# Kernel tuning notes

Measured on AMD Instinct MI355X. Metric: run time of the kernel, lower is better.

The kernel has to match this reference:

```python
import jax, jax.numpy as jnp
import numpy as np

UNITS = 50

def setup_inputs() -> dict:
    key = jax.random.key(0)
    ks = jax.random.split(key, 6)
    B, T, F = 4096, 128, 64
    scale = 0.1
    return {
        "x": jax.random.normal(ks[0], (B, T, F), dtype=jnp.float32),
        "W": jax.random.normal(ks[1], (F, 3 * UNITS), dtype=jnp.float32) * scale,
        "U": jax.random.normal(ks[2], (UNITS, 3 * UNITS), dtype=jnp.float32) * scale,
        "b": jax.random.normal(ks[3], (2, 3 * UNITS), dtype=jnp.float32) * scale,
        "Wd": jax.random.normal(ks[4], (UNITS, 1), dtype=jnp.float32) * scale,
        "bd": jnp.zeros((1,), dtype=jnp.float32),
    }

def reference(x, W, U, b, Wd, bd):
    # Keras GRU, reset_after=True, activation=relu, recurrent_activation=sigmoid.
    B, T, F = x.shape
    u = UNITS
    # Precompute input projections for all timesteps: [B,T,3u]
    xp = jnp.einsum('btf,fk->btk', x, W) + b[0]
    xp = jnp.moveaxis(xp, 1, 0)  # [T,B,3u]
    bi = b[1]

    def step(h, xt):
        hp = h @ U + bi                     # [B,3u]
        xz, xr, xh = xt[:, :u], xt[:, u:2*u], xt[:, 2*u:]
        hz, hr, hh = hp[:, :u], hp[:, u:2*u], hp[:, 2*u:]
        z = jax.nn.sigmoid(xz + hz)
        r = jax.nn.sigmoid(xr + hr)
        hcand = jax.nn.relu(xh + r * hh)
        h_new = z * h + (1.0 - z) * hcand
        return h_new, None

    h0 = jnp.zeros((B, u), dtype=x.dtype)
    hT, _ = jax.lax.scan(step, h0, xp)
    # Dropout is identity at inference; Dense head:
    return hT @ Wd + bd
```

## Files before the change

### kernel.cpp

```cpp
#include <hip/hip_runtime.h>
#include <math.h>

typedef _Float16 v8h __attribute__((ext_vector_type(8)));
typedef float v4f __attribute__((ext_vector_type(4)));

#define UNITS    50
#define K3       150
#define FDIM     64
#define TSTEPS   128
#define BATCH    4096
#define NBATCH   16
#define NTHREADS 192
#define HS16_STRIDE 72
#define HS32_STRIDE 52
#define SP_STRIDE   20


__global__ __launch_bounds__(NTHREADS, 1)
void gru_mfma(const float* __restrict__ x, const float* __restrict__ W,
              const float* __restrict__ U, const float* __restrict__ bias,
              const float* __restrict__ Wd, const float* __restrict__ bd,
              float* __restrict__ out) {
    __shared__ float    sPre[4 * 64 * SP_STRIDE];
    __shared__ _Float16 hs16[NBATCH * HS16_STRIDE];
    __shared__ float    hs32[NBATCH * HS32_STRIDE];

    const int tid  = threadIdx.x;
    const int g    = tid >> 6;
    const int lane = tid & 63;
    const int n    = lane & 15;
    const int quad = lane >> 4;
    const int b0   = blockIdx.x * NBATCH;

    for (int i = tid; i < NBATCH * HS16_STRIDE; i += NTHREADS) hs16[i] = (_Float16)0.f;
    for (int i = tid; i < NBATCH * HS32_STRIDE; i += NTHREADS) hs32[i] = 0.f;

    v8h B[4][4];
    #pragma unroll
    for (int kt = 0; kt < 4; ++kt) {
        #pragma unroll
        for (int nt = 0; nt < 4; ++nt) {
            const int c = nt * 16 + n;
            v8h f;
            #pragma unroll
            for (int j = 0; j < 8; ++j) {
                const int k = kt * 32 + quad * 8 + j;
                float v = 0.f;
                if (c < UNITS) {
                    const int gcol = g * UNITS + c;
                    if (k < FDIM)              v = W[k * K3 + gcol];
                    else if (k < FDIM + UNITS) v = U[(k - FDIM) * K3 + gcol];
                }
                f[j] = (_Float16)v;
            }
            B[kt][nt] = f;
        }
    }

    float bZR[4], bX[4], bH[4];
    #pragma unroll
    for (int nt = 0; nt < 4; ++nt) {
        const int c = nt * 16 + n;
        float vzr = 0.f, vx = 0.f, vh = 0.f;
        if (c < UNITS) {
            if (g < 2) vzr = bias[g * UNITS + c] + bias[K3 + g * UNITS + c];
            vx = bias[2 * UNITS + c];
            vh = bias[K3 + 2 * UNITS + c];
        }
        bZR[nt] = vzr; bX[nt] = vx; bH[nt] = vh;
    }

    const float* xbase = x + ((size_t)(b0 + n) * TSTEPS) * FDIM + quad * 8;
    v4f px0 = *(const v4f*)(xbase + 0);
    v4f px1 = *(const v4f*)(xbase + 4);
    v4f px2 = *(const v4f*)(xbase + 32);
    v4f px3 = *(const v4f*)(xbase + 36);

    __syncthreads();

    for (int t = 0; t < TSTEPS; ++t) {
        v8h A0, A1, A2, A3;
        #pragma unroll
        for (int j = 0; j < 4; ++j) {
            A0[j]     = (_Float16)px0[j];
            A0[j + 4] = (_Float16)px1[j];
            A1[j]     = (_Float16)px2[j];
            A1[j + 4] = (_Float16)px3[j];
        }
        A2 = *(const v8h*)(&hs16[n * HS16_STRIDE + quad * 8]);
        A3 = *(const v8h*)(&hs16[n * HS16_STRIDE + 32 + quad * 8]);

        if (t + 1 < TSTEPS) {
            const float* xp = xbase + (size_t)(t + 1) * FDIM;
            px0 = *(const v4f*)(xp + 0);
            px1 = *(const v4f*)(xp + 4);
            px2 = *(const v4f*)(xp + 32);
            px3 = *(const v4f*)(xp + 36);
        }

        if (g < 2) {
            #pragma unroll
            for (int nt = 0; nt < 4; ++nt) {
                v4f acc = {bZR[nt], bZR[nt], bZR[nt], bZR[nt]};
                acc = __builtin_amdgcn_mfma_f32_16x16x32_f16(A0, B[0][nt], acc, 0, 0, 0);
                acc = __builtin_amdgcn_mfma_f32_16x16x32_f16(A1, B[1][nt], acc, 0, 0, 0);
                acc = __builtin_amdgcn_mfma_f32_16x16x32_f16(A2, B[2][nt], acc, 0, 0, 0);
                acc = __builtin_amdgcn_mfma_f32_16x16x32_f16(A3, B[3][nt], acc, 0, 0, 0);
                const int c = nt * 16 + n;
                *(v4f*)(&sPre[(g * 64 + c) * SP_STRIDE + quad * 4]) = acc;
            }
        } else {
            #pragma unroll
            for (int nt = 0; nt < 4; ++nt) {
                v4f ax = {bX[nt], bX[nt], bX[nt], bX[nt]};
                ax = __builtin_amdgcn_mfma_f32_16x16x32_f16(A0, B[0][nt], ax, 0, 0, 0);
                ax = __builtin_amdgcn_mfma_f32_16x16x32_f16(A1, B[1][nt], ax, 0, 0, 0);
                v4f ah = {bH[nt], bH[nt], bH[nt], bH[nt]};
                ah = __builtin_amdgcn_mfma_f32_16x16x32_f16(A2, B[2][nt], ah, 0, 0, 0);
                ah = __builtin_amdgcn_mfma_f32_16x16x32_f16(A3, B[3][nt], ah, 0, 0, 0);
                const int c = nt * 16 + n;
                *(v4f*)(&sPre[(2 * 64 + c) * SP_STRIDE + quad * 4]) = ax;
                *(v4f*)(&sPre[(3 * 64 + c) * SP_STRIDE + quad * 4]) = ah;
            }
        }
        __syncthreads();

        for (int idx = tid; idx < NBATCH * UNITS; idx += NTHREADS) {
            const int u = idx >> 4;
            const int m = idx & 15;
            const float zp = sPre[(0 * 64 + u) * SP_STRIDE + m];
            const float rp = sPre[(1 * 64 + u) * SP_STRIDE + m];
            const float hx = sPre[(2 * 64 + u) * SP_STRIDE + m];
            const float hh = sPre[(3 * 64 + u) * SP_STRIDE + m];
            const float z  = 1.f / (1.f + __expf(-zp));
            const float r  = 1.f / (1.f + __expf(-rp));
            const float hc = fmaxf(fmaf(r, hh, hx), 0.f);
            const float ho = hs32[m * HS32_STRIDE + u];
            const float hn = fmaf(z, ho - hc, hc);
            hs32[m * HS32_STRIDE + u] = hn;
            hs16[m * HS16_STRIDE + u] = (_Float16)hn;
        }
        __syncthreads();
    }

    if (tid < NBATCH) {
        float acc = bd[0];
        #pragma unroll
        for (int u = 0; u < UNITS; ++u)
            acc = fmaf(hs32[tid * HS32_STRIDE + u], Wd[u], acc);
        out[b0 + tid] = acc;
    }
}

extern "C" void kernel_launch(void* const* d_in, const int* in_sizes, int n_in,
                              void* d_out, int out_size, void* d_ws, size_t ws_size,
                              hipStream_t stream) {
    const float* x    = (const float*)d_in[0];
    const float* W    = (const float*)d_in[1];
    const float* U    = (const float*)d_in[2];
    const float* bias = (const float*)d_in[3];
    const float* Wd   = (const float*)d_in[4];
    const float* bd   = (const float*)d_in[5];
    float* out = (float*)d_out;

    dim3 grid(BATCH / NBATCH);
    dim3 block(NTHREADS);
    gru_mfma<<<grid, block, 0, stream>>>(x, W, U, bias, Wd, bd, out);
}
```

Baseline: 308.3 us.

## Run each GRU batch tile in a single wave with register-resident gates

Collapses the three-wave block into one 64-lane wave that computes all z, r and h gate MFMAs and applies the GRU update directly on the accumulator registers. This removes the shared-memory pre-activation staging and one barrier per timestep. The hidden state now stays in fp32 registers, and the recurrent h-bias is folded into the weight matrix through a constant-one column in the fp16 state. The sigmoids use exp2 and a single shared reciprocal. The trade-off is roughly three times more MFMA work per wave and many more weight registers (48 v8h), which risks register pressure and longer serial MFMA chains per block.

```diff
diff --git a/kernel.cpp b/kernel.cpp
--- a/kernel.cpp
+++ b/kernel.cpp
@@ -9,77 +9,97 @@
 #define FDIM     64
 #define TSTEPS   128
 #define BATCH    4096
-#define NBATCH   16
-#define NTHREADS 192
-#define HS16_STRIDE 72
-#define HS32_STRIDE 52
-#define SP_STRIDE   20
+#define NB       16
+#define H16S     72
+#define H32S     52
 
+#if __has_builtin(__builtin_amdgcn_exp2f)
+__device__ __forceinline__ float fast_exp2(float x) { return __builtin_amdgcn_exp2f(x); }
+#else
+__device__ __forceinline__ float fast_exp2(float x) { return exp2f(x); }
+#endif
+#if __has_builtin(__builtin_amdgcn_rcpf)
+__device__ __forceinline__ float fast_rcp(float x) { return __builtin_amdgcn_rcpf(x); }
+#else
+__device__ __forceinline__ float fast_rcp(float x) { return 1.0f / x; }
+#endif
 
-__global__ __launch_bounds__(NTHREADS, 1)
-void gru_mfma(const float* __restrict__ x, const float* __restrict__ W,
-              const float* __restrict__ U, const float* __restrict__ bias,
+__global__ __launch_bounds__(64, 1)
+void gru_wave(const float* __restrict__ x, const float* __restrict__ W,
+              const float* __restrict__ U, const float* __restrict__ bv,
               const float* __restrict__ Wd, const float* __restrict__ bd,
               float* __restrict__ out) {
-    __shared__ float    sPre[4 * 64 * SP_STRIDE];
-    __shared__ _Float16 hs16[NBATCH * HS16_STRIDE];
-    __shared__ float    hs32[NBATCH * HS32_STRIDE];
+    __shared__ _Float16 hs16[NB * H16S];
+    __shared__ float    hs32[NB * H32S];
 
-    const int tid  = threadIdx.x;
-    const int g    = tid >> 6;
-    const int lane = tid & 63;
+    const int lane = threadIdx.x;
     const int n    = lane & 15;
     const int quad = lane >> 4;
-    const int b0   = blockIdx.x * NBATCH;
+    const int b0   = blockIdx.x * NB;
 
-    for (int i = tid; i < NBATCH * HS16_STRIDE; i += NTHREADS) hs16[i] = (_Float16)0.f;
-    for (int i = tid; i < NBATCH * HS32_STRIDE; i += NTHREADS) hs32[i] = 0.f;
+    for (int i = lane; i < NB * H16S; i += 64) hs16[i] = (_Float16)0.f;
+    __syncthreads();
+    if (lane < NB) hs16[lane * H16S + 50] = (_Float16)1.f;
 
-    v8h B[4][4];
+    v8h Bz[4][4], Br[4][4], Bh[4][4];
     #pragma unroll
     for (int kt = 0; kt < 4; ++kt) {
         #pragma unroll
         for (int nt = 0; nt < 4; ++nt) {
             const int c = nt * 16 + n;
-            v8h f;
+            v8h fz, fr, fh;
             #pragma unroll
             for (int j = 0; j < 8; ++j) {
                 const int k = kt * 32 + quad * 8 + j;
-                float v = 0.f;
+                float vz = 0.f, vr = 0.f, vh = 0.f;
                 if (c < UNITS) {
-                    const int gcol = g * UNITS + c;
-                    if (k < FDIM)              v = W[k * K3 + gcol];
-                    else if (k < FDIM + UNITS) v = U[(k - FDIM) * K3 + gcol];
+                    if (k < FDIM) {
+                        vz = W[k * K3 + c];
+                        vr = W[k * K3 + 50 + c];
+                        vh = W[k * K3 + 100 + c];
+                    } else if (k < FDIM + UNITS) {
+                        const int ur = k - FDIM;
+                        vz = U[ur * K3 + c];
+                        vr = U[ur * K3 + 50 + c];
+                        vh = U[ur * K3 + 100 + c];
+                    } else if (k == FDIM + UNITS) {
+                        vh = bv[250 + c];
+                    }
                 }
-                f[j] = (_Float16)v;
+                fz[j] = (_Float16)vz; fr[j] = (_Float16)vr; fh[j] = (_Float16)vh;
             }
-            B[kt][nt] = f;
+            Bz[kt][nt] = fz; Br[kt][nt] = fr; Bh[kt][nt] = fh;
         }
     }
 
-    float bZR[4], bX[4], bH[4];
+    const float CE = -1.44269504f;
+    float bzc[4], brc[4], bx4[4];
     #pragma unroll
     for (int nt = 0; nt < 4; ++nt) {
         const int c = nt * 16 + n;
-        float vzr = 0.f, vx = 0.f, vh = 0.f;
+        float z = 0.f, r = 0.f, xb = 0.f;
         if (c < UNITS) {
-            if (g < 2) vzr = bias[g * UNITS + c] + bias[K3 + g * UNITS + c];
-            vx = bias[2 * UNITS + c];
-            vh = bias[K3 + 2 * UNITS + c];
+            z  = CE * (bv[c]       + bv[150 + c]);
+            r  = CE * (bv[50 + c]  + bv[200 + c]);
+            xb = bv[100 + c];
         }
-        bZR[nt] = vzr; bX[nt] = vx; bH[nt] = vh;
+        bzc[nt] = z; brc[nt] = r; bx4[nt] = xb;
     }
 
-    const float* xbase = x + ((size_t)(b0 + n) * TSTEPS) * FDIM + quad * 8;
-    v4f px0 = *(const v4f*)(xbase + 0);
-    v4f px1 = *(const v4f*)(xbase + 4);
-    v4f px2 = *(const v4f*)(xbase + 32);
-    v4f px3 = *(const v4f*)(xbase + 36);
+    v4f h32[4];
+    #pragma unroll
+    for (int nt = 0; nt < 4; ++nt) h32[nt] = (v4f){0.f, 0.f, 0.f, 0.f};
+
+    const float* xb = x + ((size_t)(b0 + n) * TSTEPS) * FDIM + quad * 8;
+    v4f px0 = *(const v4f*)(xb + 0);
+    v4f px1 = *(const v4f*)(xb + 4);
+    v4f px2 = *(const v4f*)(xb + 32);
+    v4f px3 = *(const v4f*)(xb + 36);
 
     __syncthreads();
 
     for (int t = 0; t < TSTEPS; ++t) {
-        v8h A0, A1, A2, A3;
+        v8h A0, A1;
         #pragma unroll
         for (int j = 0; j < 4; ++j) {
             A0[j]     = (_Float16)px0[j];
@@ -87,68 +107,72 @@
             A1[j]     = (_Float16)px2[j];
             A1[j + 4] = (_Float16)px3[j];
         }
-        A2 = *(const v8h*)(&hs16[n * HS16_STRIDE + quad * 8]);
-        A3 = *(const v8h*)(&hs16[n * HS16_STRIDE + 32 + quad * 8]);
+        v8h A2 = *(const v8h*)(&hs16[n * H16S + quad * 8]);
+        v8h A3 = *(const v8h*)(&hs16[n * H16S + 32 + quad * 8]);
 
         if (t + 1 < TSTEPS) {
-            const float* xp = xbase + (size_t)(t + 1) * FDIM;
+            const float* xp = xb + (size_t)(t + 1) * FDIM;
             px0 = *(const v4f*)(xp + 0);
             px1 = *(const v4f*)(xp + 4);
             px2 = *(const v4f*)(xp + 32);
             px3 = *(const v4f*)(xp + 36);
         }
 
-        if (g < 2) {
+        const v4f zero4 = (v4f){0.f, 0.f, 0.f, 0.f};
+        #pragma unroll
+        for (int nt = 0; nt < 4; ++nt) {
+            v4f az = __builtin_amdgcn_mfma_f32_16x16x32_f16(A0, Bz[0][nt], zero4, 0, 0, 0);
+            az     = __builtin_amdgcn_mfma_f32_16x16x32_f16(A1, Bz[1][nt], az,    0, 0, 0);
+            v4f ar = __builtin_amdgcn_mfma_f32_16x16x32_f16(A0, Br[0][nt], zero4, 0, 0, 0);
+            ar     = __builtin_amdgcn_mfma_f32_16x16x32_f16(A1, Br[1][nt], ar,    0, 0, 0);
+            v4f ax = __builtin_amdgcn_mfma_f32_16x16x32_f16(A0, Bh[0][nt], zero4, 0, 0, 0);
+            ax     = __builtin_amdgcn_mfma_f32_16x16x32_f16(A1, Bh[1][nt], ax,    0, 0, 0);
+            az     = __builtin_amdgcn_mfma_f32_16x16x32_f16(A2, Bz[2][nt], az,    0, 0, 0);
+            az     = __builtin_amdgcn_mfma_f32_16x16x32_f16(A3, Bz[3][nt], az,    0, 0, 0);
+            ar     = __builtin_amdgcn_mfma_f32_16x16x32_f16(A2, Br[2][nt], ar,    0, 0, 0);
+            ar     = __builtin_amdgcn_mfma_f32_16x16x32_f16(A3, Br[3][nt], ar,    0, 0, 0);
+            v4f ah = __builtin_amdgcn_mfma_f32_16x16x32_f16(A2, Bh[2][nt], zero4, 0, 0, 0);
+            ah     = __builtin_amdgcn_mfma_f32_16x16x32_f16(A3, Bh[3][nt], ah,    0, 0, 0);
+
             #pragma unroll
-            for (int nt = 0; nt < 4; ++nt) {
-                v4f acc = {bZR[nt], bZR[nt], bZR[nt], bZR[nt]};
-                acc = __builtin_amdgcn_mfma_f32_16x16x32_f16(A0, B[0][nt], acc, 0, 0, 0);
-                acc = __builtin_amdgcn_mfma_f32_16x16x32_f16(A1, B[1][nt], acc, 0, 0, 0);
-                acc = __builtin_amdgcn_mfma_f32_16x16x32_f16(A2, B[2][nt], acc, 0, 0, 0);
-                acc = __builtin_amdgcn_mfma_f32_16x16x32_f16(A3, B[3][nt], acc, 0, 0, 0);
+            for (int r = 0; r < 4; ++r) {
+                const float ez = fast_exp2(fmaf(az[r], CE, bzc[nt]));
+                const float er = fast_exp2(fmaf(ar[r], CE, brc[nt]));
+                const float pz = 1.f + ez;
+                const float pr = 1.f + er;
+                const float d  = fast_rcp(pz * pr);
+                const float zg = d * pr;
+                const float rg = d * pz;
+                const float hx = ax[r] + bx4[nt];
+                const float hc = fmaxf(fmaf(rg, ah[r], hx), 0.f);
+                const float ho = h32[nt][r];
+                const float hn = fmaf(zg, ho - hc, hc);
+                h32[nt][r] = hn;
                 const int c = nt * 16 + n;
-                *(v4f*)(&sPre[(g * 64 + c) * SP_STRIDE + quad * 4]) = acc;
+                if (nt < 3 || n < 2) {
+                    hs16[(quad * 4 + r) * H16S + c] = (_Float16)hn;
+                }
             }
-        } else {
-            #pragma unroll
-            for (int nt = 0; nt < 4; ++nt) {
-                v4f ax = {bX[nt], bX[nt], bX[nt], bX[nt]};
-                ax = __builtin_amdgcn_mfma_f32_16x16x32_f16(A0, B[0][nt], ax, 0, 0, 0);
-                ax = __builtin_amdgcn_mfma_f32_16x16x32_f16(A1, B[1][nt], ax, 0, 0, 0);
-                v4f ah = {bH[nt], bH[nt], bH[nt], bH[nt]};
-                ah = __builtin_amdgcn_mfma_f32_16x16x32_f16(A2, B[2][nt], ah, 0, 0, 0);
-                ah = __builtin_amdgcn_mfma_f32_16x16x32_f16(A3, B[3][nt], ah, 0, 0, 0);
-                const int c = nt * 16 + n;
-                *(v4f*)(&sPre[(2 * 64 + c) * SP_STRIDE + quad * 4]) = ax;
-                *(v4f*)(&sPre[(3 * 64 + c) * SP_STRIDE + quad * 4]) = ah;
-            }
-        }
-        __syncthreads();
-
-        for (int idx = tid; idx < NBATCH * UNITS; idx += NTHREADS) {
-            const int u = idx >> 4;
-            const int m = idx & 15;
-            const float zp = sPre[(0 * 64 + u) * SP_STRIDE + m];
-            const float rp = sPre[(1 * 64 + u) * SP_STRIDE + m];
-            const float hx = sPre[(2 * 64 + u) * SP_STRIDE + m];
-            const float hh = sPre[(3 * 64 + u) * SP_STRIDE + m];
-            const float z  = 1.f / (1.f + __expf(-zp));
-            const float r  = 1.f / (1.f + __expf(-rp));
-            const float hc = fmaxf(fmaf(r, hh, hx), 0.f);
-            const float ho = hs32[m * HS32_STRIDE + u];
-            const float hn = fmaf(z, ho - hc, hc);
-            hs32[m * HS32_STRIDE + u] = hn;
-            hs16[m * HS16_STRIDE + u] = (_Float16)hn;
         }
         __syncthreads();
     }
 
-    if (tid < NBATCH) {
+    #pragma unroll
+    for (int nt = 0; nt < 4; ++nt) {
+        const int c = nt * 16 + n;
+        if (c < UNITS) {
+            #pragma unroll
+            for (int r = 0; r < 4; ++r)
+                hs32[(quad * 4 + r) * H32S + c] = h32[nt][r];
+        }
+    }
+    __syncthreads();
+    if (lane < NB) {
         float acc = bd[0];
         #pragma unroll
         for (int u = 0; u < UNITS; ++u)
-            acc = fmaf(hs32[tid * HS32_STRIDE + u], Wd[u], acc);
-        out[b0 + tid] = acc;
+            acc = fmaf(hs32[lane * H32S + u], Wd[u], acc);
+        out[b0 + lane] = acc;
     }
 }
 
@@ -158,12 +182,12 @@
     const float* x    = (const float*)d_in[0];
     const float* W    = (const float*)d_in[1];
     const float* U    = (const float*)d_in[2];
-    const float* bias = (const float*)d_in[3];
+    const float* bv   = (const float*)d_in[3];
     const float* Wd   = (const float*)d_in[4];
     const float* bd   = (const float*)d_in[5];
     float* out = (float*)d_out;
 
-    dim3 grid(BATCH / NBATCH);
-    dim3 block(NTHREADS);
-    gru_mfma<<<grid, block, 0, stream>>>(x, W, U, bias, Wd, bd, out);
+    dim3 grid(BATCH / NB);
+    dim3 block(64);
+    gru_wave<<<grid, block, 0, stream>>>(x, W, U, bv, Wd, bd, out);
 }
```

Measured after the change: 356.0 us. 1.15x slower.
